# Performance work log

Measured on AMD Instinct MI355X. Metric: run time of the kernel, lower is better.

The kernel has to match this reference:

```python
import jax, jax.numpy as jnp
import numpy as np

DIMENSIONS = 1100
NUM_LEVELS = 256
SIZE = 28
BATCH = 512


def _build_level_table(num_levels, d):
    # Thermometer-style level codes, exactly as in Encoder.__init__
    c = d // num_levels
    r = d % num_levels
    levels = []
    for number in range(num_levels):
        if number == 0:
            my_list = [-1] * d
        elif number == num_levels - 1:
            my_list = [1] * d
        else:
            mm = [-1] * (num_levels - number) + [1] * number
            my_list = []
            for _ in range(c):
                my_list = mm + my_list
            if r != 0:
                my_list = mm[-r:] + my_list
        levels.append(my_list)
    return np.asarray(levels, dtype=np.float32)  # (256, 1100)


def setup_inputs() -> dict:
    key = jax.random.key(0)
    k1, k2 = jax.random.split(key)
    # pixel intensities in [0, 255]
    x = jax.random.uniform(k1, (BATCH, SIZE, SIZE), dtype=jnp.float32) * 255.0
    # bipolar +-1 position hypervectors (stands in for LFSR-generated sequence)
    position_weight = jnp.where(
        jax.random.bernoulli(k2, 0.5, (SIZE * SIZE, DIMENSIONS)), 1.0, -1.0
    ).astype(jnp.float32)
    value_weight = jnp.asarray(_build_level_table(NUM_LEVELS, DIMENSIONS))
    return {"x": x, "position_weight": position_weight, "value_weight": value_weight}


def reference(x, position_weight, value_weight):
    B = x.shape[0]
    xf = x.reshape(B, -1)  # (B, N) flatten
    num = value_weight.shape[0]
    # torchhd Level: map value in [low=0, high=256] to level index
    idx = jnp.round(jnp.clip(xf / 256.0, 0.0, 1.0) * (num - 1)).astype(jnp.int32)
    # bind: elementwise multiply of gathered level HVs with position HVs -> (B, N, D)
    bound = value_weight[idx] * position_weight[None, :, :]
    # multiset: sum over positions -> (B, D)
    s = bound.sum(axis=1)
    # sign threshold
    return jnp.where(s > 0, jnp.float32(1.0), jnp.float32(-1.0))
```

## Files before the change

kernel.cpp:

```cpp
#include <hip/hip_runtime.h>
#include <cstdint>

#define DIMS   1100
#define NPOS   784
#define NLEV   256
#define BATCH  512
#define NW     25
#define TROW   260

__global__ __launch_bounds__(256) void prep_kernel(
    const float* __restrict__ pos, const float* __restrict__ val,
    int* __restrict__ t_arr, uint32_t* __restrict__ pbits)
{
    int job = blockIdx.x * 256 + threadIdx.x;
    if (job < DIMS) {
        int d = job;
        int cnt = 0;
        for (int l = 0; l < NLEV; ++l)
            cnt += (val[l * DIMS + d] < 0.0f) ? 1 : 0;
        t_arr[d] = cnt;
    } else if (job < DIMS + NW * DIMS) {
        int j = job - DIMS;
        int w = j / DIMS;
        int d = j - w * DIMS;
        int n0 = w * 32;
        int nmax = NPOS - n0; if (nmax > 32) nmax = 32;
        uint32_t bits = 0;
        for (int i = 0; i < nmax; ++i)
            bits |= (pos[(n0 + i) * DIMS + d] > 0.0f ? 1u : 0u) << i;
        pbits[w * DIMS + d] = bits;
    }
}

__global__ __launch_bounds__(256) void encode_kernel(
    const float* __restrict__ x, const int* __restrict__ t_arr,
    const uint32_t* __restrict__ pbits, float* __restrict__ out)
{
    __shared__ uint32_t U[NW * TROW];
    __shared__ uint32_t S[NW * 8];

    const int tid = threadIdx.x;
    const int b = blockIdx.x;

    uint4* U4 = (uint4*)U;
    #pragma unroll
    for (int i = 0; i < (NW * TROW / 4 + 255) / 256; ++i) {
        int p = tid + i * 256;
        if (p < NW * TROW / 4) U4[p] = make_uint4(0u, 0u, 0u, 0u);
    }
    __syncthreads();

    for (int n = tid; n < NPOS; n += 256) {
        float v = x[b * NPOS + n] * (1.0f / 256.0f);
        v = fminf(fmaxf(v, 0.0f), 1.0f) * 255.0f;
        int idx = (int)rintf(v);
        atomicOr(&U[(n >> 5) * TROW + idx], 1u << (n & 31));
    }
    __syncthreads();

    const int w = tid & 31;
    const int seg = tid >> 5;
    if (w < NW) {
        uint4* row4 = (uint4*)&U[w * TROW + seg * 32];
        uint32_t rr[32];
        #pragma unroll
        for (int i = 0; i < 8; ++i) {
            uint4 t4 = row4[i];
            rr[4*i+0] = t4.x; rr[4*i+1] = t4.y; rr[4*i+2] = t4.z; rr[4*i+3] = t4.w;
        }
        uint32_t acc = 0;
        #pragma unroll
        for (int k = 31; k >= 0; --k) { acc |= rr[k]; rr[k] = acc; }
        #pragma unroll
        for (int i = 0; i < 8; ++i)
            row4[i] = make_uint4(rr[4*i+0], rr[4*i+1], rr[4*i+2], rr[4*i+3]);
        S[w * 8 + seg] = acc;
    }
    __syncthreads();
    if (w < NW) {
        uint32_t carry = 0;
        for (int s2 = seg + 1; s2 < 8; ++s2) carry |= S[w * 8 + s2];
        if (carry) {
            uint4* row4 = (uint4*)&U[w * TROW + seg * 32];
            #pragma unroll
            for (int i = 0; i < 8; ++i) {
                uint4 r = row4[i];
                r.x |= carry; r.y |= carry; r.z |= carry; r.w |= carry;
                row4[i] = r;
            }
        }
    }
    __syncthreads();

    #pragma unroll
    for (int k = 0; k < 5; ++k) {
        int d = tid + (k << 8);
        if (d < DIMS) {
            int td = t_arr[d];
            uint32_t diff = 0;
            #pragma unroll
            for (int ww = 0; ww < NW; ++ww) {
                uint32_t pb = pbits[ww * DIMS + d];
                uint32_t ub = U[ww * TROW + td];
                diff += __popc(pb ^ ub);
            }
            out[b * DIMS + d] = (diff < (NPOS / 2)) ? 1.0f : -1.0f;
        }
    }
}

extern "C" void kernel_launch(void* const* d_in, const int* in_sizes, int n_in,
                              void* d_out, int out_size, void* d_ws, size_t ws_size,
                              hipStream_t stream) {
    const float* x   = (const float*)d_in[0];
    const float* pos = (const float*)d_in[1];
    const float* val = (const float*)d_in[2];
    float* out = (float*)d_out;

    int* t_arr = (int*)d_ws;
    uint32_t* pbits = (uint32_t*)d_ws + 1104;

    const int prep_jobs = DIMS + NW * DIMS;
    prep_kernel<<<(prep_jobs + 255) / 256, 256, 0, stream>>>(pos, val, t_arr, pbits);
    encode_kernel<<<BATCH, 256, 0, stream>>>(x, t_arr, pbits, out);
}
```

Measured before the change: 85.30 us.

## Parallelize preprocessing with wave ballots and streamline encode shared-memory passes

```diff
diff --git a/kernel.cpp b/kernel.cpp
--- a/kernel.cpp
+++ b/kernel.cpp
@@ -6,30 +6,34 @@
 #define NLEV   256
 #define BATCH  512
 #define NW     25
-#define TROW   260
+#define TROW   268
 
-__global__ __launch_bounds__(256) void prep_kernel(
+__global__ __launch_bounds__(256) void prep2_kernel(
     const float* __restrict__ pos, const float* __restrict__ val,
     int* __restrict__ t_arr, uint32_t* __restrict__ pbits)
 {
-    int job = blockIdx.x * 256 + threadIdx.x;
-    if (job < DIMS) {
-        int d = job;
-        int cnt = 0;
-        for (int l = 0; l < NLEV; ++l)
-            cnt += (val[l * DIMS + d] < 0.0f) ? 1 : 0;
-        t_arr[d] = cnt;
-    } else if (job < DIMS + NW * DIMS) {
-        int j = job - DIMS;
-        int w = j / DIMS;
-        int d = j - w * DIMS;
-        int n0 = w * 32;
-        int nmax = NPOS - n0; if (nmax > 32) nmax = 32;
-        uint32_t bits = 0;
-        for (int i = 0; i < nmax; ++i)
-            bits |= (pos[(n0 + i) * DIMS + d] > 0.0f ? 1u : 0u) << i;
-        pbits[w * DIMS + d] = bits;
+    const int d    = blockIdx.x;
+    const int tid  = threadIdx.x;
+    const int lane = tid & 63;
+    const int wv   = tid >> 6;
+    __shared__ int s4[4];
+
+    bool neg = val[tid * DIMS + d] < 0.0f;
+    unsigned long long m = __ballot(neg);
+    if (lane == 0) s4[wv] = __popcll(m);
+
+    #pragma unroll
+    for (int p = 0; p < 4; ++p) {
+        int n = p * 256 + tid;
+        bool bit = (n < NPOS) ? (pos[n * DIMS + d] > 0.0f) : false;
+        unsigned long long mm = __ballot(bit);
+        int w0 = p * 8 + wv * 2;
+        if (lane == 0 && w0 < NW)      pbits[w0 * DIMS + d]       = (uint32_t)mm;
+        if (lane == 32 && w0 + 1 < NW) pbits[(w0 + 1) * DIMS + d] = (uint32_t)(mm >> 32);
     }
+
+    __syncthreads();
+    if (tid == 0) t_arr[d] = s4[0] + s4[1] + s4[2] + s4[3];
 }
 
 __global__ __launch_bounds__(256) void encode_kernel(
@@ -42,51 +46,58 @@
     const int tid = threadIdx.x;
     const int b = blockIdx.x;
 
+    int td0[5];
+    #pragma unroll
+    for (int k = 0; k < 5; ++k) {
+        int d = tid + (k << 8);
+        td0[k] = (d < DIMS) ? t_arr[d] : 0;
+    }
+
     uint4* U4 = (uint4*)U;
     #pragma unroll
-    for (int i = 0; i < (NW * TROW / 4 + 255) / 256; ++i) {
+    for (int i = 0; i < 7; ++i) {
         int p = tid + i * 256;
         if (p < NW * TROW / 4) U4[p] = make_uint4(0u, 0u, 0u, 0u);
     }
     __syncthreads();
 
-    for (int n = tid; n < NPOS; n += 256) {
-        float v = x[b * NPOS + n] * (1.0f / 256.0f);
-        v = fminf(fmaxf(v, 0.0f), 1.0f) * 255.0f;
-        int idx = (int)rintf(v);
-        atomicOr(&U[(n >> 5) * TROW + idx], 1u << (n & 31));
+    if (tid < NPOS / 4) {
+        float4 xv = ((const float4*)x)[b * (NPOS / 4) + tid];
+        float vv[4] = {xv.x, xv.y, xv.z, xv.w};
+        #pragma unroll
+        for (int j = 0; j < 4; ++j) {
+            int n = tid * 4 + j;
+            float v = fminf(fmaxf(vv[j] * (1.0f / 256.0f), 0.0f), 1.0f) * 255.0f;
+            int idx = (int)rintf(v);
+            atomicOr(&U[(n >> 5) * TROW + idx], 1u << (n & 31));
+        }
     }
     __syncthreads();
 
-    const int w = tid & 31;
-    const int seg = tid >> 5;
-    if (w < NW) {
+    if (tid < NW * 8) {
+        const int w = tid >> 3, seg = tid & 7;
         uint4* row4 = (uint4*)&U[w * TROW + seg * 32];
-        uint32_t rr[32];
-        #pragma unroll
-        for (int i = 0; i < 8; ++i) {
-            uint4 t4 = row4[i];
-            rr[4*i+0] = t4.x; rr[4*i+1] = t4.y; rr[4*i+2] = t4.z; rr[4*i+3] = t4.w;
-        }
         uint32_t acc = 0;
         #pragma unroll
-        for (int k = 31; k >= 0; --k) { acc |= rr[k]; rr[k] = acc; }
-        #pragma unroll
-        for (int i = 0; i < 8; ++i)
-            row4[i] = make_uint4(rr[4*i+0], rr[4*i+1], rr[4*i+2], rr[4*i+3]);
-        S[w * 8 + seg] = acc;
+        for (int i = 7; i >= 0; --i) {
+            uint4 t = row4[i];
+            uint32_t d3 = acc | t.w, d2 = d3 | t.z, d1 = d2 | t.y, d0 = d1 | t.x;
+            row4[i] = make_uint4(d0, d1, d2, d3);
+            acc = d0;
+        }
+        S[tid] = acc;
     }
     __syncthreads();
-    if (w < NW) {
+    if (tid < NW * 8) {
+        const int w = tid >> 3, seg = tid & 7;
         uint32_t carry = 0;
-        for (int s2 = seg + 1; s2 < 8; ++s2) carry |= S[w * 8 + s2];
+        for (int s2 = seg + 1; s2 < 8; ++s2) carry |= S[(w << 3) + s2];
         if (carry) {
             uint4* row4 = (uint4*)&U[w * TROW + seg * 32];
             #pragma unroll
             for (int i = 0; i < 8; ++i) {
                 uint4 r = row4[i];
-                r.x |= carry; r.y |= carry; r.z |= carry; r.w |= carry;
-                row4[i] = r;
+                row4[i] = make_uint4(r.x | carry, r.y | carry, r.z | carry, r.w | carry);
             }
         }
     }
@@ -96,12 +107,12 @@
     for (int k = 0; k < 5; ++k) {
         int d = tid + (k << 8);
         if (d < DIMS) {
-            int td = t_arr[d];
+            int t = td0[k];
             uint32_t diff = 0;
             #pragma unroll
             for (int ww = 0; ww < NW; ++ww) {
                 uint32_t pb = pbits[ww * DIMS + d];
-                uint32_t ub = U[ww * TROW + td];
+                uint32_t ub = U[ww * TROW + t];
                 diff += __popc(pb ^ ub);
             }
             out[b * DIMS + d] = (diff < (NPOS / 2)) ? 1.0f : -1.0f;
@@ -120,7 +131,6 @@
     int* t_arr = (int*)d_ws;
     uint32_t* pbits = (uint32_t*)d_ws + 1104;
 
-    const int prep_jobs = DIMS + NW * DIMS;
-    prep_kernel<<<(prep_jobs + 255) / 256, 256, 0, stream>>>(pos, val, t_arr, pbits);
+    prep2_kernel<<<DIMS, 256, 0, stream>>>(pos, val, t_arr, pbits);
     encode_kernel<<<BATCH, 256, 0, stream>>>(x, t_arr, pbits, out);
 }
```

Result: faster. 77.25 us (-9.4%).
